# Performance work log

Measured on AMD Instinct MI355X. Metric: run time of the kernel, lower is better.

## Reference

```python
import jax, jax.numpy as jnp
import numpy as np

N_NODES = 50000
N_EDGES = 1250000
DIM = 64
NUM_CLASS = 10
NUM_GRAPHS = 256


def setup_inputs() -> dict:
    key = jax.random.key(0)
    ks = jax.random.split(key, 12)
    node_embeddings = jax.random.normal(ks[0], (N_NODES, DIM), dtype=jnp.float32)
    edge_index = jax.random.randint(ks[1], (2, N_EDGES), 0, N_NODES, dtype=jnp.int32)
    batch = jnp.sort(jax.random.randint(ks[2], (N_NODES,), 0, NUM_GRAPHS, dtype=jnp.int32))
    s = 1.0 / np.sqrt(2 * DIM)
    W1 = jax.random.normal(ks[3], (2 * DIM, DIM), dtype=jnp.float32) * s
    b1 = jnp.zeros((DIM,), dtype=jnp.float32)
    W2 = jax.random.normal(ks[4], (2 * DIM, DIM), dtype=jnp.float32) * s
    b2 = jnp.zeros((DIM,), dtype=jnp.float32)
    sd = 1.0 / np.sqrt(DIM)
    Wd1 = jax.random.normal(ks[5], (DIM, DIM), dtype=jnp.float32) * sd
    bd1 = jnp.zeros((DIM,), dtype=jnp.float32)
    Wd2 = jax.random.normal(ks[6], (DIM, NUM_CLASS), dtype=jnp.float32) * sd
    bd2 = jnp.zeros((NUM_CLASS,), dtype=jnp.float32)
    return {
        "node_embeddings": node_embeddings,
        "edge_index": edge_index,
        "batch": batch,
        "W1": W1, "b1": b1, "W2": W2, "b2": b2,
        "Wd1": Wd1, "bd1": bd1, "Wd2": Wd2, "bd2": bd2,
    }


def sage_conv(x, edge_index, W, b):
    # GraphSAGE conv with sum aggregation:
    # gather source node features, sum-scatter into destination nodes,
    # then linear on concat(self, aggregated).
    src, dst = edge_index[0], edge_index[1]
    msgs = x[src]  # [E, d] irregular gather
    agg = jax.ops.segment_sum(msgs, dst, num_segments=x.shape[0])  # [N, d]
    h = jnp.concatenate([x, agg], axis=-1)  # [N, 2d]
    return h @ W + b


def reference(node_embeddings, edge_index, batch,
              W1, b1, W2, b2, Wd1, bd1, Wd2, bd2):
    x = jax.nn.relu(sage_conv(node_embeddings, edge_index, W1, b1))
    x = jax.nn.relu(sage_conv(x, edge_index, W2, b2))
    # batch_read_out: sum-pool node features per graph -> [num_graphs, d]
    g = jax.ops.segment_sum(x, batch, num_segments=NUM_GRAPHS)
    g = jax.nn.relu(g @ Wd1 + bd1)
    # dropout inactive (inference / predict path)
    logits = g @ Wd2 + bd2
    return jax.nn.softmax(logits, axis=-1)
```

## Files before the change

### kernel.cpp

```cpp
#include <hip/hip_runtime.h>

#define N_NODES 50000
#define N_EDGES 1250000
#define DIM 64
#define NUM_CLASS 10
#define NUM_GRAPHS 256
#define CAP 64
#define BSHIFT 6
#define NB ((N_NODES + 63) / 64)
#define BCAP 2048
#define I4_TOTAL (N_EDGES / 4)
#define I4_PER_BLOCK 4096

typedef __attribute__((ext_vector_type(8))) short short8v;
typedef __attribute__((ext_vector_type(4))) float float4v;
typedef __attribute__((ext_vector_type(2))) float float2v;

#if defined(__has_builtin)
#if __has_builtin(__builtin_amdgcn_cvt_pk_f32_fp8) && __has_builtin(__builtin_amdgcn_cvt_pk_fp8_f32)
#define HW_FP8 1
#endif
#endif

__device__ inline unsigned f2e4m3_sw(float x) {
    float af = fabsf(x);
    unsigned s = (__float_as_uint(x) >> 31) << 7;
    if (af >= 448.f) return s | 0x7E;
    if (af < 0.015625f) {
        int n = (int)rintf(af * 512.f);
        if (n >= 8) return s | 0x08;
        return s | (unsigned)n;
    }
    unsigned u = __float_as_uint(af);
    u += 0x7FFFF + ((u >> 20) & 1);
    int e32 = (int)(u >> 23) - 127;
    if (e32 > 8) return s | 0x7E;
    unsigned m = (u >> 20) & 7;
    return s | ((unsigned)(e32 + 7) << 3) | m;
}

__device__ inline float e4m3f_sw(unsigned b) {
    unsigned e = (b >> 3) & 15;
    unsigned nz = e ? 1u : 0u;
    float mant = (float)((b & 7) + (nz << 3));
    float v = ldexpf(mant, (int)e - 9 - (int)nz);
    return (b & 0x80) ? -v : v;
}

__device__ inline float4 dec4(unsigned q) {
#ifdef HW_FP8
    float2v lo = __builtin_amdgcn_cvt_pk_f32_fp8(q, false);
    float2v hi = __builtin_amdgcn_cvt_pk_f32_fp8(q, true);
    return make_float4(lo.x, lo.y, hi.x, hi.y);
#else
    return make_float4(e4m3f_sw(q & 0xff), e4m3f_sw((q >> 8) & 0xff),
                       e4m3f_sw((q >> 16) & 0xff), e4m3f_sw(q >> 24));
#endif
}

__device__ inline unsigned enc4(float a, float b, float c, float d) {
#ifdef HW_FP8
    int u = __builtin_amdgcn_cvt_pk_fp8_f32(a, b, 0, false);
    u = __builtin_amdgcn_cvt_pk_fp8_f32(c, d, u, true);
    return (unsigned)u;
#else
    return f2e4m3_sw(a) | (f2e4m3_sw(b) << 8) | (f2e4m3_sw(c) << 16) | (f2e4m3_sw(d) << 24);
#endif
}

__device__ inline unsigned char enc1(float a) {
#ifdef HW_FP8
    return (unsigned char)(__builtin_amdgcn_cvt_pk_fp8_f32(a, a, 0, false) & 0xff);
#else
    return (unsigned char)f2e4m3_sw(a);
#endif
}

__global__ __launch_bounds__(512) void bucket_kernel(
    const int4* __restrict__ src4, const int4* __restrict__ dst4,
    int* __restrict__ bcount, unsigned int* __restrict__ bdata)
{
    __shared__ int hist[NB];
    __shared__ int base[NB];
    const int tid = threadIdx.x;
    for (int k = tid; k < NB; k += 512) hist[k] = 0;
    __syncthreads();

    const int i4base = blockIdx.x * I4_PER_BLOCK;
    const int i4end = min(i4base + I4_PER_BLOCK, I4_TOTAL);

    for (int idx = i4base + tid; idx < i4end; idx += 512) {
        int4 d = dst4[idx];
        atomicAdd(&hist[d.x >> BSHIFT], 1);
        atomicAdd(&hist[d.y >> BSHIFT], 1);
        atomicAdd(&hist[d.z >> BSHIFT], 1);
        atomicAdd(&hist[d.w >> BSHIFT], 1);
    }
    __syncthreads();

    for (int k = tid; k < NB; k += 512) {
        int c = hist[k];
        base[k] = c ? atomicAdd(&bcount[k], c) : 0;
        hist[k] = 0;
    }
    __syncthreads();

    for (int idx = i4base + tid; idx < i4end; idx += 512) {
        int4 s = src4[idx];
        int4 d = dst4[idx];
        int k, p;
        k = d.x >> BSHIFT; p = base[k] + atomicAdd(&hist[k], 1);
        if (p < BCAP) bdata[(size_t)k * BCAP + p] = ((unsigned)(d.x & 63) << 16) | (unsigned)s.x;
        k = d.y >> BSHIFT; p = base[k] + atomicAdd(&hist[k], 1);
        if (p < BCAP) bdata[(size_t)k * BCAP + p] = ((unsigned)(d.y & 63) << 16) | (unsigned)s.y;
        k = d.z >> BSHIFT; p = base[k] + atomicAdd(&hist[k], 1);
        if (p < BCAP) bdata[(size_t)k * BCAP + p] = ((unsigned)(d.z & 63) << 16) | (unsigned)s.z;
        k = d.w >> BSHIFT; p = base[k] + atomicAdd(&hist[k], 1);
        if (p < BCAP) bdata[(size_t)k * BCAP + p] = ((unsigned)(d.w & 63) << 16) | (unsigned)s.w;
    }
}

__global__ __launch_bounds__(256) void csr_build_kernel(
    const int* __restrict__ bcount, const unsigned int* __restrict__ bdata,
    int* __restrict__ deg, unsigned short* __restrict__ csr)
{
    __shared__ unsigned short lcsr[64 * CAP];
    __shared__ int ldeg[64];
    const int tid = threadIdx.x;
    const int bk = blockIdx.x;
    if (tid < 64) ldeg[tid] = 0;
    __syncthreads();

    const int cnt = min(bcount[bk], BCAP);
    for (int i = tid; i < cnt; i += 256) {
        unsigned int e = bdata[(size_t)bk * BCAP + i];
        int d = (int)(e >> 16);
        int p = atomicAdd(&ldeg[d], 1);
        if (p < CAP) lcsr[d * CAP + p] = (unsigned short)(e & 0xffff);
    }
    __syncthreads();

    const int node0 = bk << BSHIFT;
    const int nlocal = min(64, N_NODES - node0);
    uint4* csr16 = (uint4*)(csr + (size_t)node0 * CAP);
    const uint4* l16 = (const uint4*)lcsr;
    for (int i = tid; i < nlocal * 8; i += 256) csr16[i] = l16[i];
    if (tid < nlocal) deg[node0 + tid] = ldeg[tid];
}

__global__ __launch_bounds__(256) void prep_kernel(
    const float4* __restrict__ x04, const float* __restrict__ W1,
    const float* __restrict__ W2, unsigned* __restrict__ x0q,
    unsigned short* __restrict__ WB, int* __restrict__ bcount)
{
    const int bid = blockIdx.x;
    const int tid = threadIdx.x;
    if (bid < 3125) {
        int t = bid * 256 + tid;
        float4 v = x04[t];
        x0q[t] = enc4(v.x, v.y, v.z, v.w);
    } else if (bid < 3253) {
        int t = (bid - 3125) * 256 + tid;
        int layer = t >> 14;
        int r = t & 16383;
        int i    = r & 7;
        int lane = (r >> 3) & 63;
        int h    = (r >> 9) & 1;
        int ct   = (r >> 10) & 3;
        int kt   = (r >> 12) & 3;
        int k   = kt * 32 + (lane >> 4) * 8 + i;
        int col = ct * 16 + (lane & 15);
        const float* W = layer ? W2 : W1;
        float x = W[k * 64 + col];
        unsigned bits = __float_as_uint(x);
        unsigned short u;
        if (h == 0) {
            u = (unsigned short)(bits >> 16);
        } else {
            float y = x - __uint_as_float(bits & 0xffff0000u);
            u = (unsigned short)(__float_as_uint(y) >> 16);
        }
        WB[t] = u;
    } else {
        for (int k = tid; k < NB; k += 256) bcount[k] = 0;
    }
}

__global__ __launch_bounds__(256) void sage_layer_kernel(
    const float4* __restrict__ x4,
    const unsigned* __restrict__ xq,
    const int* __restrict__ deg,
    const unsigned short* __restrict__ csr,
    const unsigned short* __restrict__ WB,
    const float* __restrict__ b,
    float* __restrict__ out,
    unsigned char* __restrict__ outq)
{
    __shared__ float hT[128][33];

    const int tid = threadIdx.x;
    const int g = tid >> 4;
    const int c = tid & 15;
    const int n0 = blockIdx.x * 32;

    #pragma unroll
    for (int p = 0; p < 2; ++p) {
        const int nl = g + p * 16;
        const int n = n0 + nl;
        float4 xv = make_float4(0.f, 0.f, 0.f, 0.f);
        float4 aggv = make_float4(0.f, 0.f, 0.f, 0.f);
        if (n < N_NODES) {
            xv = x4[(size_t)n * 16 + c];
            const int dcount = min(deg[n], CAP);
            const unsigned short* row = csr + (size_t)n * CAP;
            int j = 0;
            for (; j + 8 <= dcount; j += 8) {
                ushort4 sa = *(const ushort4*)(row + j);
                ushort4 sb = *(const ushort4*)(row + j + 4);
                unsigned q0 = xq[(size_t)sa.x * 16 + c];
                unsigned q1 = xq[(size_t)sa.y * 16 + c];
                unsigned q2 = xq[(size_t)sa.z * 16 + c];
                unsigned q3 = xq[(size_t)sa.w * 16 + c];
                unsigned q4 = xq[(size_t)sb.x * 16 + c];
                unsigned q5 = xq[(size_t)sb.y * 16 + c];
                unsigned q6 = xq[(size_t)sb.z * 16 + c];
                unsigned q7 = xq[(size_t)sb.w * 16 + c];
                float4 f0 = dec4(q0), f1 = dec4(q1), f2 = dec4(q2), f3 = dec4(q3);
                float4 f4 = dec4(q4), f5 = dec4(q5), f6 = dec4(q6), f7 = dec4(q7);
                aggv.x += (f0.x + f1.x) + (f2.x + f3.x) + (f4.x + f5.x) + (f6.x + f7.x);
                aggv.y += (f0.y + f1.y) + (f2.y + f3.y) + (f4.y + f5.y) + (f6.y + f7.y);
                aggv.z += (f0.z + f1.z) + (f2.z + f3.z) + (f4.z + f5.z) + (f6.z + f7.z);
                aggv.w += (f0.w + f1.w) + (f2.w + f3.w) + (f4.w + f5.w) + (f6.w + f7.w);
            }
            for (; j < dcount; ++j) {
                int s = row[j];
                float4 f = dec4(xq[(size_t)s * 16 + c]);
                aggv.x += f.x; aggv.y += f.y; aggv.z += f.z; aggv.w += f.w;
            }
        }
        hT[4 * c + 0][nl] = xv.x;
        hT[4 * c + 1][nl] = xv.y;
        hT[4 * c + 2][nl] = xv.z;
        hT[4 * c + 3][nl] = xv.w;
        hT[64 + 4 * c + 0][nl] = aggv.x;
        hT[64 + 4 * c + 1][nl] = aggv.y;
        hT[64 + 4 * c + 2][nl] = aggv.z;
        hT[64 + 4 * c + 3][nl] = aggv.w;
    }
    __syncthreads();

    const int lane = tid & 63;
    const int wid  = tid >> 6;
    const int rt   = wid >> 1;
    const int ct0  = (wid & 1) * 2;
    const int r  = lane & 15;
    const int q  = lane >> 4;

    const int col0 = (ct0 + 0) * 16 + r;
    const int col1 = (ct0 + 1) * 16 + r;
    const float bv0 = b[col0];
    const float bv1 = b[col1];
    float4v acc0 = {bv0, bv0, bv0, bv0};
    float4v acc1 = {bv1, bv1, bv1, bv1};

    #pragma unroll
    for (int kt = 0; kt < 4; ++kt) {
        short8v a_hi, a_lo;
        #pragma unroll
        for (int i = 0; i < 8; ++i) {
            float av = hT[kt * 32 + q * 8 + i][rt * 16 + r];
            unsigned bits = __float_as_uint(av);
            a_hi[i] = (short)(bits >> 16);
            float y = av - __uint_as_float(bits & 0xffff0000u);
            a_lo[i] = (short)(__float_as_uint(y) >> 16);
        }
        const unsigned short* Wk = WB + kt * 4096;
        const short8v bh0 = *(const short8v*)(Wk + (ct0 + 0) * 1024 + 0 * 512 + lane * 8);
        const short8v bl0 = *(const short8v*)(Wk + (ct0 + 0) * 1024 + 1 * 512 + lane * 8);
        const short8v bh1 = *(const short8v*)(Wk + (ct0 + 1) * 1024 + 0 * 512 + lane * 8);
        const short8v bl1 = *(const short8v*)(Wk + (ct0 + 1) * 1024 + 1 * 512 + lane * 8);

        acc0 = __builtin_amdgcn_mfma_f32_16x16x32_bf16(a_hi, bh0, acc0, 0, 0, 0);
        acc0 = __builtin_amdgcn_mfma_f32_16x16x32_bf16(a_hi, bl0, acc0, 0, 0, 0);
        acc0 = __builtin_amdgcn_mfma_f32_16x16x32_bf16(a_lo, bh0, acc0, 0, 0, 0);
        acc1 = __builtin_amdgcn_mfma_f32_16x16x32_bf16(a_hi, bh1, acc1, 0, 0, 0);
        acc1 = __builtin_amdgcn_mfma_f32_16x16x32_bf16(a_hi, bl1, acc1, 0, 0, 0);
        acc1 = __builtin_amdgcn_mfma_f32_16x16x32_bf16(a_lo, bh1, acc1, 0, 0, 0);
    }

    #pragma unroll
    for (int reg = 0; reg < 4; ++reg) {
        int n = n0 + rt * 16 + q * 4 + reg;
        if (n < N_NODES) {
            float v0 = fmaxf(acc0[reg], 0.f);
            float v1 = fmaxf(acc1[reg], 0.f);
            out[(size_t)n * 64 + col0] = v0;
            out[(size_t)n * 64 + col1] = v1;
            if (outq) {
                outq[(size_t)n * 64 + col0] = enc1(v0);
                outq[(size_t)n * 64 + col1] = enc1(v1);
            }
        }
    }
}

__global__ __launch_bounds__(256) void readout_kernel(
    const float* __restrict__ x,
    const int* __restrict__ batch,
    const float* __restrict__ Wd1,
    const float* __restrict__ bd1,
    const float* __restrict__ Wd2,
    const float* __restrict__ bd2,
    float* __restrict__ out)
{
    __shared__ float part[4][64];
    __shared__ float grow[64];
    __shared__ float h1[64];
    __shared__ float logits[NUM_CLASS];

    const int g = blockIdx.x;
    const int tid = threadIdx.x;
    const int d = tid & 63;
    const int r = tid >> 6;

    int lo = 0, hi = N_NODES;
    while (lo < hi) { int mid = (lo + hi) >> 1; if (batch[mid] < g) lo = mid + 1; else hi = mid; }
    const int start = lo;
    hi = N_NODES;
    while (lo < hi) { int mid = (lo + hi) >> 1; if (batch[mid] < g + 1) lo = mid + 1; else hi = mid; }
    const int end = lo;

    float acc = 0.f;
    for (int n = start + r; n < end; n += 4) acc += x[(size_t)n * 64 + d];
    part[r][d] = acc;
    __syncthreads();

    if (tid < 64) {
        grow[d] = part[0][d] + part[1][d] + part[2][d] + part[3][d];
    }
    __syncthreads();

    if (tid < 64) {
        float a = bd1[d];
        #pragma unroll 8
        for (int k = 0; k < 64; ++k) a += grow[k] * Wd1[k * 64 + d];
        h1[d] = fmaxf(a, 0.f);
    }
    __syncthreads();

    if (tid < NUM_CLASS) {
        float a = bd2[tid];
        #pragma unroll 8
        for (int k = 0; k < 64; ++k) a += h1[k] * Wd2[k * 10 + tid];
        logits[tid] = a;
    }
    __syncthreads();

    if (tid < NUM_CLASS) {
        float m = logits[0];
        #pragma unroll
        for (int i = 1; i < NUM_CLASS; ++i) m = fmaxf(m, logits[i]);
        float s = 0.f;
        #pragma unroll
        for (int i = 0; i < NUM_CLASS; ++i) s += expf(logits[i] - m);
        out[g * NUM_CLASS + tid] = expf(logits[tid] - m) / s;
    }
}

extern "C" void kernel_launch(void* const* d_in, const int* in_sizes, int n_in,
                              void* d_out, int out_size, void* d_ws, size_t ws_size,
                              hipStream_t stream) {
    const float* x0   = (const float*)d_in[0];
    const int*   edge = (const int*)d_in[1];
    const int*   batch= (const int*)d_in[2];
    const float* W1   = (const float*)d_in[3];
    const float* b1   = (const float*)d_in[4];
    const float* W2   = (const float*)d_in[5];
    const float* b2   = (const float*)d_in[6];
    const float* Wd1  = (const float*)d_in[7];
    const float* bd1  = (const float*)d_in[8];
    const float* Wd2  = (const float*)d_in[9];
    const float* bd2  = (const float*)d_in[10];
    float* out = (float*)d_out;

    const int* src = edge;
    const int* dst = edge + N_EDGES;

    const size_t nodeBytes = (size_t)N_NODES * DIM * sizeof(float);
    const size_t nodeBytesQ = (size_t)N_NODES * DIM;
    char* ws = (char*)d_ws;
    float* B   = (float*)ws;            ws += nodeBytes;
    float* C   = (float*)ws;            ws += nodeBytes;
    int*   deg = (int*)ws;              ws += N_NODES * 4;
    unsigned short* csr = (unsigned short*)ws; ws += (size_t)N_NODES * CAP * 2;
    int*   bcount = (int*)ws;           ws += NB * 4;
    unsigned short* WB = (unsigned short*)ws;  ws += 32768 * 2;
    unsigned char* Bq = (unsigned char*)ws;    ws += nodeBytesQ;
    unsigned int*  bdata = (unsigned int*)C;
    unsigned*      x0q   = (unsigned*)((char*)C + (8 << 20));

    const int bucketBlocks = (I4_TOTAL + I4_PER_BLOCK - 1) / I4_PER_BLOCK;
    const int nodeBlocks = (N_NODES + 31) / 32;

    prep_kernel<<<3254, 256, 0, stream>>>(
        (const float4*)x0, W1, W2, x0q, WB, bcount);

    bucket_kernel<<<bucketBlocks, 512, 0, stream>>>(
        (const int4*)src, (const int4*)dst, bcount, bdata);
    csr_build_kernel<<<NB, 256, 0, stream>>>(bcount, bdata, deg, csr);

    sage_layer_kernel<<<nodeBlocks, 256, 0, stream>>>(
        (const float4*)x0, x0q, deg, csr, WB, b1, B, Bq);
    sage_layer_kernel<<<nodeBlocks, 256, 0, stream>>>(
        (const float4*)B, (const unsigned*)Bq, deg, csr, WB + 16384, b2, C, nullptr);

    readout_kernel<<<NUM_GRAPHS, 256, 0, stream>>>(
        C, batch, Wd1, bd1, Wd2, bd2, out);
}
```

Baseline: 106.3 us.

## Fuse graph sum-pooling into second SAGE layer and store layer-1 output as bf16

The second SAGE layer now writes no node features. Each block stages its ReLU output in LDS, runs segmented sums over the sorted batch ids, and atomically adds the partial graph sums into a zeroed per-graph buffer. A small MLP kernel then reads only that buffer. The layer-1 self features are stored as bf16 instead of fp32, which cuts write and read traffic. In exchange this adds float atomics with a nondeterministic summation order, and bf16 self features lose precision.

```diff
diff --git a/kernel.cpp b/kernel.cpp
--- a/kernel.cpp
+++ b/kernel.cpp
@@ -22,6 +22,14 @@
 #endif
 #endif
 
+__device__ inline unsigned short f2bf_rne(float f) {
+    unsigned b = __float_as_uint(f);
+    return (unsigned short)((b + 0x7fff + ((b >> 16) & 1)) >> 16);
+}
+__device__ inline float bf2f(unsigned short u) {
+    return __uint_as_float((unsigned)u << 16);
+}
+
 __device__ inline unsigned f2e4m3_sw(float x) {
     float af = fabsf(x);
     unsigned s = (__float_as_uint(x) >> 31) << 7;
@@ -38,7 +46,6 @@
     unsigned m = (u >> 20) & 7;
     return s | ((unsigned)(e32 + 7) << 3) | m;
 }
-
 __device__ inline float e4m3f_sw(unsigned b) {
     unsigned e = (b >> 3) & 15;
     unsigned nz = e ? 1u : 0u;
@@ -57,7 +64,6 @@
                        e4m3f_sw((q >> 16) & 0xff), e4m3f_sw(q >> 24));
 #endif
 }
-
 __device__ inline unsigned enc4(float a, float b, float c, float d) {
 #ifdef HW_FP8
     int u = __builtin_amdgcn_cvt_pk_fp8_f32(a, b, 0, false);
@@ -67,7 +73,6 @@
     return f2e4m3_sw(a) | (f2e4m3_sw(b) << 8) | (f2e4m3_sw(c) << 16) | (f2e4m3_sw(d) << 24);
 #endif
 }
-
 __device__ inline unsigned char enc1(float a) {
 #ifdef HW_FP8
     return (unsigned char)(__builtin_amdgcn_cvt_pk_fp8_f32(a, a, 0, false) & 0xff);
@@ -151,7 +156,8 @@
 __global__ __launch_bounds__(256) void prep_kernel(
     const float4* __restrict__ x04, const float* __restrict__ W1,
     const float* __restrict__ W2, unsigned* __restrict__ x0q,
-    unsigned short* __restrict__ WB, int* __restrict__ bcount)
+    unsigned short* __restrict__ WB, int* __restrict__ bcount,
+    float* __restrict__ G)
 {
     const int bid = blockIdx.x;
     const int tid = threadIdx.x;
@@ -183,20 +189,25 @@
         WB[t] = u;
     } else {
         for (int k = tid; k < NB; k += 256) bcount[k] = 0;
+        for (int k = tid; k < NUM_GRAPHS * DIM; k += 256) G[k] = 0.f;
     }
 }
 
 __global__ __launch_bounds__(256) void sage_layer_kernel(
-    const float4* __restrict__ x4,
+    const float4* __restrict__ xs4,
+    const ushort4* __restrict__ xsb,
     const unsigned* __restrict__ xq,
     const int* __restrict__ deg,
     const unsigned short* __restrict__ csr,
     const unsigned short* __restrict__ WB,
     const float* __restrict__ b,
-    float* __restrict__ out,
-    unsigned char* __restrict__ outq)
+    unsigned short* __restrict__ outb,
+    unsigned char* __restrict__ outq,
+    float* __restrict__ G,
+    const int* __restrict__ batch)
 {
     __shared__ float hT[128][33];
+    __shared__ int batch_lds[32];
 
     const int tid = threadIdx.x;
     const int g = tid >> 4;
@@ -210,7 +221,12 @@
         float4 xv = make_float4(0.f, 0.f, 0.f, 0.f);
         float4 aggv = make_float4(0.f, 0.f, 0.f, 0.f);
         if (n < N_NODES) {
-            xv = x4[(size_t)n * 16 + c];
+            if (xs4) {
+                xv = xs4[(size_t)n * 16 + c];
+            } else {
+                ushort4 u = xsb[(size_t)n * 16 + c];
+                xv = make_float4(bf2f(u.x), bf2f(u.y), bf2f(u.z), bf2f(u.w));
+            }
             const int dcount = min(deg[n], CAP);
             const unsigned short* row = csr + (size_t)n * CAP;
             int j = 0;
@@ -288,82 +304,86 @@
         acc1 = __builtin_amdgcn_mfma_f32_16x16x32_bf16(a_lo, bh1, acc1, 0, 0, 0);
     }
 
-    #pragma unroll
-    for (int reg = 0; reg < 4; ++reg) {
-        int n = n0 + rt * 16 + q * 4 + reg;
-        if (n < N_NODES) {
-            float v0 = fmaxf(acc0[reg], 0.f);
-            float v1 = fmaxf(acc1[reg], 0.f);
-            out[(size_t)n * 64 + col0] = v0;
-            out[(size_t)n * 64 + col1] = v1;
-            if (outq) {
+    if (G == nullptr) {
+        #pragma unroll
+        for (int reg = 0; reg < 4; ++reg) {
+            int n = n0 + rt * 16 + q * 4 + reg;
+            if (n < N_NODES) {
+                float v0 = fmaxf(acc0[reg], 0.f);
+                float v1 = fmaxf(acc1[reg], 0.f);
+                outb[(size_t)n * 64 + col0] = f2bf_rne(v0);
+                outb[(size_t)n * 64 + col1] = f2bf_rne(v1);
                 outq[(size_t)n * 64 + col0] = enc1(v0);
                 outq[(size_t)n * 64 + col1] = enc1(v1);
             }
         }
-    }
-}
-
-__global__ __launch_bounds__(256) void readout_kernel(
-    const float* __restrict__ x,
-    const int* __restrict__ batch,
+    } else {
+        __syncthreads();
+        float* outLds = (float*)hT;
+        #pragma unroll
+        for (int reg = 0; reg < 4; ++reg) {
+            int lr = rt * 16 + q * 4 + reg;
+            outLds[lr * 66 + col0] = fmaxf(acc0[reg], 0.f);
+            outLds[lr * 66 + col1] = fmaxf(acc1[reg], 0.f);
+        }
+        if (tid < 32) batch_lds[tid] = (n0 + tid < N_NODES) ? batch[n0 + tid] : -1;
+        __syncthreads();
+        if (tid < 64) {
+            int prev = -1; float acc = 0.f;
+            for (int rr = 0; rr < 32; ++rr) {
+                int bg = batch_lds[rr];
+                if (bg < 0) break;
+                if (bg != prev) {
+                    if (prev >= 0) unsafeAtomicAdd(&G[prev * 64 + tid], acc);
+                    acc = 0.f; prev = bg;
+                }
+                acc += outLds[rr * 66 + tid];
+            }
+            if (prev >= 0) unsafeAtomicAdd(&G[prev * 64 + tid], acc);
+        }
+    }
+}
+
+__global__ __launch_bounds__(64) void mlp_kernel(
+    const float* __restrict__ G,
     const float* __restrict__ Wd1,
     const float* __restrict__ bd1,
     const float* __restrict__ Wd2,
     const float* __restrict__ bd2,
     float* __restrict__ out)
 {
-    __shared__ float part[4][64];
     __shared__ float grow[64];
     __shared__ float h1[64];
     __shared__ float logits[NUM_CLASS];
 
-    const int g = blockIdx.x;
-    const int tid = threadIdx.x;
-    const int d = tid & 63;
-    const int r = tid >> 6;
-
-    int lo = 0, hi = N_NODES;
-    while (lo < hi) { int mid = (lo + hi) >> 1; if (batch[mid] < g) lo = mid + 1; else hi = mid; }
-    const int start = lo;
-    hi = N_NODES;
-    while (lo < hi) { int mid = (lo + hi) >> 1; if (batch[mid] < g + 1) lo = mid + 1; else hi = mid; }
-    const int end = lo;
-
-    float acc = 0.f;
-    for (int n = start + r; n < end; n += 4) acc += x[(size_t)n * 64 + d];
-    part[r][d] = acc;
-    __syncthreads();
-
-    if (tid < 64) {
-        grow[d] = part[0][d] + part[1][d] + part[2][d] + part[3][d];
-    }
-    __syncthreads();
-
-    if (tid < 64) {
-        float a = bd1[d];
+    const int gI = blockIdx.x;
+    const int d = threadIdx.x;
+
+    grow[d] = G[gI * 64 + d];
+    __syncthreads();
+
+    float a = bd1[d];
+    #pragma unroll 8
+    for (int k = 0; k < 64; ++k) a += grow[k] * Wd1[k * 64 + d];
+    h1[d] = fmaxf(a, 0.f);
+    __syncthreads();
+
+    if (d < NUM_CLASS) {
+        float s = bd2[d];
         #pragma unroll 8
-        for (int k = 0; k < 64; ++k) a += grow[k] * Wd1[k * 64 + d];
-        h1[d] = fmaxf(a, 0.f);
-    }
-    __syncthreads();
-
-    if (tid < NUM_CLASS) {
-        float a = bd2[tid];
-        #pragma unroll 8
-        for (int k = 0; k < 64; ++k) a += h1[k] * Wd2[k * 10 + tid];
-        logits[tid] = a;
-    }
-    __syncthreads();
-
-    if (tid < NUM_CLASS) {
+        for (int k = 0; k < 64; ++k) s += h1[k] * Wd2[k * 10 + d];
+        logits[d] = s;
+    }
+    __syncthreads();
+
+    if (d < NUM_CLASS) {
         float m = logits[0];
         #pragma unroll
         for (int i = 1; i < NUM_CLASS; ++i) m = fmaxf(m, logits[i]);
         float s = 0.f;
         #pragma unroll
         for (int i = 0; i < NUM_CLASS; ++i) s += expf(logits[i] - m);
-        out[g * NUM_CLASS + tid] = expf(logits[tid] - m) / s;
+        out[gI * NUM_CLASS + d] = expf(logits[d] - m) / s;
     }
 }
 
@@ -386,34 +406,32 @@
     const int* src = edge;
     const int* dst = edge + N_EDGES;
 
-    const size_t nodeBytes = (size_t)N_NODES * DIM * sizeof(float);
-    const size_t nodeBytesQ = (size_t)N_NODES * DIM;
     char* ws = (char*)d_ws;
-    float* B   = (float*)ws;            ws += nodeBytes;
-    float* C   = (float*)ws;            ws += nodeBytes;
-    int*   deg = (int*)ws;              ws += N_NODES * 4;
+    int*   deg = (int*)ws;                     ws += N_NODES * 4;
     unsigned short* csr = (unsigned short*)ws; ws += (size_t)N_NODES * CAP * 2;
-    int*   bcount = (int*)ws;           ws += NB * 4;
+    int*   bcount = (int*)ws;                  ws += NB * 4;
     unsigned short* WB = (unsigned short*)ws;  ws += 32768 * 2;
-    unsigned char* Bq = (unsigned char*)ws;    ws += nodeBytesQ;
-    unsigned int*  bdata = (unsigned int*)C;
-    unsigned*      x0q   = (unsigned*)((char*)C + (8 << 20));
+    float* G = (float*)ws;                     ws += NUM_GRAPHS * DIM * 4;
+    unsigned* x0q = (unsigned*)ws;             ws += (size_t)N_NODES * 16 * 4;
+    unsigned short* Bb = (unsigned short*)ws;  ws += (size_t)N_NODES * DIM * 2;
+    unsigned char* Bq = (unsigned char*)ws;    ws += (size_t)N_NODES * DIM;
+    unsigned int* bdata = (unsigned int*)ws;   ws += (size_t)NB * BCAP * 4;
 
     const int bucketBlocks = (I4_TOTAL + I4_PER_BLOCK - 1) / I4_PER_BLOCK;
     const int nodeBlocks = (N_NODES + 31) / 32;
 
     prep_kernel<<<3254, 256, 0, stream>>>(
-        (const float4*)x0, W1, W2, x0q, WB, bcount);
+        (const float4*)x0, W1, W2, x0q, WB, bcount, G);
 
     bucket_kernel<<<bucketBlocks, 512, 0, stream>>>(
         (const int4*)src, (const int4*)dst, bcount, bdata);
     csr_build_kernel<<<NB, 256, 0, stream>>>(bcount, bdata, deg, csr);
 
     sage_layer_kernel<<<nodeBlocks, 256, 0, stream>>>(
-        (const float4*)x0, x0q, deg, csr, WB, b1, B, Bq);
+        (const float4*)x0, nullptr, x0q, deg, csr, WB, b1, Bb, Bq, nullptr, nullptr);
     sage_layer_kernel<<<nodeBlocks, 256, 0, stream>>>(
-        (const float4*)B, (const unsigned*)Bq, deg, csr, WB + 16384, b2, C, nullptr);
-
-    readout_kernel<<<NUM_GRAPHS, 256, 0, stream>>>(
-        C, batch, Wd1, bd1, Wd2, bd2, out);
-}
+        nullptr, (const ushort4*)Bb, (const unsigned*)Bq, deg, csr, WB + 16384, b2,
+        nullptr, nullptr, G, batch);
+
+    mlp_kernel<<<NUM_GRAPHS, 64, 0, stream>>>(G, Wd1, bd1, Wd2, bd2, out);
+}
```

After: 94.86 us (median of 2 runs). 1.12x faster.
